# Optimization experiments

Hardware: AMD Instinct MI355X
Metric: run time of the kernel (lower is better)

## Reference

```python
import jax, jax.numpy as jnp
import numpy as np


def setup_inputs() -> dict:
    key = jax.random.key(0)
    k1, k2, k3, k4 = jax.random.split(key, 4)
    TOKENS, IN_F, OUT_F = 4096, 4096, 11008
    x = jax.random.normal(k1, (TOKENS, IN_F), dtype=jnp.float32)
    # int8-valued weights stored in fp32 buffer, as in the torch module
    quantized_weight = jax.random.randint(k2, (OUT_F, IN_F), -128, 128).astype(jnp.float32)
    # per-output-channel scales, positive, small (like max|w|/127)
    weight_scales = (jax.random.uniform(k3, (OUT_F, 1), dtype=jnp.float32) * 0.03 + 0.001)
    bias = jax.random.normal(k4, (OUT_F,), dtype=jnp.float32)
    return {"x": x, "quantized_weight": quantized_weight,
            "weight_scales": weight_scales, "bias": bias}


def reference(x, quantized_weight, weight_scales, bias):
    # dequantize: per-channel scale broadcast over in_features
    weight = quantized_weight * weight_scales  # [out, in]
    # F.linear: x @ weight.T + bias
    return jnp.dot(x, weight.T) + bias
```

## Files before the change

kernel.cpp:

```cpp
#include <hip/hip_runtime.h>
#include <hip/hip_bf16.h>


typedef __attribute__((ext_vector_type(4))) int   i32x4;
typedef __attribute__((ext_vector_type(4))) float f32x4;
typedef __attribute__((ext_vector_type(4))) unsigned int u32x4;

__device__ static inline unsigned int pack4(int q0, int q1, int q2, int q3) {
    return (unsigned)(q0 & 255) | ((unsigned)(q1 & 255) << 8) |
           ((unsigned)(q2 & 255) << 16) | ((unsigned)(q3 & 255) << 24);
}

__global__ void w_to_i8(const float* __restrict__ in,
                        u32x4* __restrict__ out, long n16) {
    const long stride = (long)gridDim.x * blockDim.x;
    for (long i = (long)blockIdx.x * blockDim.x + threadIdx.x; i < n16; i += stride) {
        const f32x4* p = reinterpret_cast<const f32x4*>(in) + i * 4;
        u32x4 o;
#pragma unroll
        for (int v = 0; v < 4; ++v) {
            f32x4 f = p[v];
            o[v] = pack4(__float2int_rn(f[0]), __float2int_rn(f[1]),
                         __float2int_rn(f[2]), __float2int_rn(f[3]));
        }
        out[i] = o;
    }
}

__global__ void x_quant_i8(const float* __restrict__ x,
                           unsigned int* __restrict__ xq,
                           float* __restrict__ sx, int K) {
    const int row = blockIdx.x;
    const int tid = threadIdx.x;
    const float* xr = x + (size_t)row * K;
    float m = 0.f;
    for (int b = tid * 16; b < K; b += blockDim.x * 16) {
        const f32x4* p = (const f32x4*)(xr + b);
#pragma unroll
        for (int v = 0; v < 4; ++v) {
            f32x4 f = p[v];
            m = fmaxf(m, fmaxf(fmaxf(fabsf(f[0]), fabsf(f[1])),
                               fmaxf(fabsf(f[2]), fabsf(f[3]))));
        }
    }
#pragma unroll
    for (int off = 32; off; off >>= 1) m = fmaxf(m, __shfl_xor(m, off));
    __shared__ float red[8];
    if ((tid & 63) == 0) red[tid >> 6] = m;
    __syncthreads();
    const int nw = blockDim.x >> 6;
    m = red[0];
    for (int i = 1; i < nw; ++i) m = fmaxf(m, red[i]);
    const float inv = (m > 0.f) ? 127.0f / m : 0.f;
    if (tid == 0) sx[row] = m * (1.0f / 127.0f);
    for (int b = tid * 16; b < K; b += blockDim.x * 16) {
        const f32x4* p = (const f32x4*)(xr + b);
        u32x4 o;
#pragma unroll
        for (int v = 0; v < 4; ++v) {
            f32x4 f = p[v];
            int q0 = min(127, max(-127, __float2int_rn(f[0] * inv)));
            int q1 = min(127, max(-127, __float2int_rn(f[1] * inv)));
            int q2 = min(127, max(-127, __float2int_rn(f[2] * inv)));
            int q3 = min(127, max(-127, __float2int_rn(f[3] * inv)));
            o[v] = pack4(q0, q1, q2, q3);
        }
        *reinterpret_cast<u32x4*>((char*)xq + (size_t)row * K + b) = o;
    }
}


#define GLOAD16(src, dst) __builtin_amdgcn_global_load_lds( \
    (const __attribute__((address_space(1))) void*)(src),   \
    (__attribute__((address_space(3))) void*)(dst), 16, 0, 0)

#define FENCE() asm volatile("" ::: "memory")
#define BAR()  do { FENCE(); __builtin_amdgcn_s_barrier(); FENCE(); } while (0)
#define WAIT_VM(n) asm volatile("s_waitcnt vmcnt(" #n ")" ::: "memory")
#define WAIT_LGKM0() asm volatile("s_waitcnt lgkmcnt(0)" ::: "memory")
#define SCHED0() __builtin_amdgcn_sched_barrier(0)

__global__ __launch_bounds__(512, 4)
void qlinear_gemm_i8(const char* __restrict__ A,
                     const char* __restrict__ B,
                     const float* __restrict__ sx,
                     const float* __restrict__ scales,
                     const float* __restrict__ bias,
                     float* __restrict__ C,
                     int M, int N, int K, int nbx) {
    __shared__ __align__(128) char smem[73728];

    const int tid  = threadIdx.x;
    const int lane = tid & 63;
    const int wid  = tid >> 6;
    const int mslab = (wid >> 1) * 64;
    const int nslab = (wid & 1) * 64;

    const int nwg = gridDim.x;
    const int q = nwg >> 3, r = nwg & 7;
    const int xcd = blockIdx.x & 7, boff_ = blockIdx.x >> 3;
    const int swz = (xcd < r ? xcd * (q + 1) : r * (q + 1) + (xcd - r) * q) + boff_;
    const int bcol = swz % nbx;
    const int brow = swz / nbx;

    const char* Ag = A + (size_t)brow * 256 * K;
    const char* Bg = B + (size_t)bcol * 128 * K;

    const int c0 = tid, c1 = tid + 512;
    const int r0 = c0 >> 2, p0 = c0 & 3;
    const int r1 = c1 >> 2, p1 = c1 & 3;
    const size_t a0base = (size_t)r0 * K + ((p0 ^ ((r0 >> 1) & 3)) << 4);
    const size_t a1base = (size_t)r1 * K + ((p1 ^ ((r1 >> 1) & 3)) << 4);
    const size_t b0base = a0base;

    auto stageT = [&](int sl, int t) {
        const size_t ko = (size_t)t * 64;
        GLOAD16(Ag + a0base + ko, smem + sl * 16384 + c0 * 16);
        GLOAD16(Ag + a1base + ko, smem + sl * 16384 + c1 * 16);
        GLOAD16(Bg + b0base + ko, smem + 49152 + sl * 8192 + c0 * 16);
    };

    const int cph  = ((lane >> 4) ^ ((lane >> 1) & 3)) << 4;
    const int aoff = (mslab + (lane & 15)) * 64 + cph;
    const int boff = (nslab + (lane & 15)) * 64 + cph;

    i32x4 acc[4][4] = {};
    i32x4 af[4], bf[4];

    auto rdAB = [&](int sl) {
        const char* pa = smem + sl * 16384 + aoff;
#pragma unroll
        for (int mi = 0; mi < 4; ++mi) af[mi] = *(const i32x4*)(pa + mi * 1024);
        const char* pb = smem + 49152 + sl * 8192 + boff;
#pragma unroll
        for (int ni = 0; ni < 4; ++ni) bf[ni] = *(const i32x4*)(pb + ni * 1024);
    };
    auto mfma16 = [&]() {
        __builtin_amdgcn_s_setprio(1);
#pragma unroll
        for (int mi = 0; mi < 4; ++mi)
#pragma unroll
            for (int ni = 0; ni < 4; ++ni)
                acc[mi][ni] = __builtin_amdgcn_mfma_i32_16x16x64_i8(
                    af[mi], bf[ni], acc[mi][ni], 0, 0, 0);
        __builtin_amdgcn_s_setprio(0);
    };

    const int NT = K / 64;

    stageT(0, 0); stageT(1, 1);
    WAIT_VM(3); BAR();

    int sl = 0;
    for (int t = 0; t < NT - 2; ++t) {
        rdAB(sl);
        int sl2 = sl + 2; if (sl2 >= 3) sl2 -= 3;
        stageT(sl2, t + 2);
        BAR();
        WAIT_LGKM0(); SCHED0();
        mfma16();
        WAIT_VM(3);
        BAR();
        sl = (sl == 2) ? 0 : sl + 1;
    }
    rdAB(sl);
    BAR();
    WAIT_LGKM0(); SCHED0();
    mfma16();
    WAIT_VM(0);
    BAR();
    sl = (sl == 2) ? 0 : sl + 1;
    rdAB(sl);
    WAIT_LGKM0(); SCHED0();
    mfma16();

    const int lc  = lane & 15;
    const int lr4 = (lane >> 4) * 4;
    float sarr[4], barr[4];
#pragma unroll
    for (int ni = 0; ni < 4; ++ni) {
        const int n = bcol * 128 + nslab + ni * 16 + lc;
        sarr[ni] = scales[n];
        barr[ni] = bias[n];
    }
#pragma unroll
    for (int mi = 0; mi < 4; ++mi) {
        const int mb = brow * 256 + mslab + mi * 16 + lr4;
        const f32x4 sxv = *(const f32x4*)&sx[mb];
#pragma unroll
        for (int j = 0; j < 4; ++j) {
            const size_t rowoff = (size_t)(mb + j) * N;
            const float sm = sxv[j];
#pragma unroll
            for (int ni = 0; ni < 4; ++ni) {
                const int n = bcol * 128 + nslab + ni * 16 + lc;
                C[rowoff + n] = fmaf((float)acc[mi][ni][j], sm * sarr[ni], barr[ni]);
            }
        }
    }
}

__global__ void qlinear_fallback(const float* __restrict__ A,
                                 const float* __restrict__ B,
                                 const float* __restrict__ scales,
                                 const float* __restrict__ bias,
                                 float* __restrict__ C, int M, int N, int K) {
    __shared__ float As[16][17], Bs[16][17];
    const int tx = threadIdx.x, ty = threadIdx.y;
    const int row = blockIdx.y * 16 + ty;
    const int col = blockIdx.x * 16 + tx;
    float acc = 0.f;
    for (int k0 = 0; k0 < K; k0 += 16) {
        As[ty][tx] = A[(long)row * K + k0 + tx];
        Bs[ty][tx] = B[(long)(blockIdx.x * 16 + ty) * K + k0 + tx];
        __syncthreads();
#pragma unroll
        for (int kk = 0; kk < 16; ++kk) acc += As[ty][kk] * Bs[tx][kk];
        __syncthreads();
    }
    C[(long)row * N + col] = fmaf(acc, scales[col], bias[col]);
}

extern "C" void kernel_launch(void* const* d_in, const int* in_sizes, int n_in,
                              void* d_out, int out_size, void* d_ws, size_t ws_size,
                              hipStream_t stream) {
    const float* x      = (const float*)d_in[0];
    const float* w      = (const float*)d_in[1];
    const float* scales = (const float*)d_in[2];
    const float* bias   = (const float*)d_in[3];
    float* out = (float*)d_out;

    const int N = in_sizes[2];
    const int K = (int)((long)in_sizes[1] / N);
    const int M = (int)((long)in_sizes[0] / K);

    const size_t need = (size_t)M * K + (size_t)N * K + (size_t)M * 4;
    const bool ok = (ws_size >= need) && (M % 256) == 0 && (N % 128) == 0 &&
                    (K % 64) == 0 && (K / 64) >= 4 && (K % 16) == 0;

    if (ok) {
        char* xq = (char*)d_ws;
        char* wq = xq + (size_t)M * K;
        float* sxbuf = (float*)(wq + (size_t)N * K);

        x_quant_i8<<<M, 256, 0, stream>>>(x, (unsigned int*)xq, sxbuf, K);
        w_to_i8<<<2048, 256, 0, stream>>>(w, (u32x4*)wq, (long)N * K / 16);

        const int nbx = N / 128;
        const int nwg = (M / 256) * nbx;
        qlinear_gemm_i8<<<nwg, 512, 0, stream>>>(xq, wq, sxbuf, scales, bias,
                                                 out, M, N, K, nbx);
    } else {
        dim3 grid(N / 16, M / 16), blk(16, 16);
        qlinear_fallback<<<grid, blk, 0, stream>>>(x, w, scales, bias, out, M, N, K);
    }
}
```

Before: 277.9 us.

## Use 4 waves with 128x64 warp tiles and drop mid-iteration barrier

```diff
diff --git a/kernel.cpp b/kernel.cpp
--- a/kernel.cpp
+++ b/kernel.cpp
@@ -77,23 +77,21 @@
 #define FENCE() asm volatile("" ::: "memory")
 #define BAR()  do { FENCE(); __builtin_amdgcn_s_barrier(); FENCE(); } while (0)
 #define WAIT_VM(n) asm volatile("s_waitcnt vmcnt(" #n ")" ::: "memory")
-#define WAIT_LGKM0() asm volatile("s_waitcnt lgkmcnt(0)" ::: "memory")
-#define SCHED0() __builtin_amdgcn_sched_barrier(0)
-
-__global__ __launch_bounds__(512, 4)
-void qlinear_gemm_i8(const char* __restrict__ A,
-                     const char* __restrict__ B,
-                     const float* __restrict__ sx,
-                     const float* __restrict__ scales,
-                     const float* __restrict__ bias,
-                     float* __restrict__ C,
-                     int M, int N, int K, int nbx) {
+
+__global__ __launch_bounds__(256, 2)
+void qlinear_gemm_i8w(const char* __restrict__ A,
+                      const char* __restrict__ B,
+                      const float* __restrict__ sx,
+                      const float* __restrict__ scales,
+                      const float* __restrict__ bias,
+                      float* __restrict__ C,
+                      int M, int N, int K, int nbx) {
     __shared__ __align__(128) char smem[73728];
 
     const int tid  = threadIdx.x;
     const int lane = tid & 63;
     const int wid  = tid >> 6;
-    const int mslab = (wid >> 1) * 64;
+    const int mslab = (wid >> 1) * 128;
     const int nslab = (wid & 1) * 64;
 
     const int nwg = gridDim.x;
@@ -106,39 +104,48 @@
     const char* Ag = A + (size_t)brow * 256 * K;
     const char* Bg = B + (size_t)bcol * 128 * K;
 
-    const int c0 = tid, c1 = tid + 512;
-    const int r0 = c0 >> 2, p0 = c0 & 3;
-    const int r1 = c1 >> 2, p1 = c1 & 3;
-    const size_t a0base = (size_t)r0 * K + ((p0 ^ ((r0 >> 1) & 3)) << 4);
-    const size_t a1base = (size_t)r1 * K + ((p1 ^ ((r1 >> 1) & 3)) << 4);
-    const size_t b0base = a0base;
+    size_t ga[4], gb[2];
+#pragma unroll
+    for (int j = 0; j < 4; ++j) {
+        const int c = tid + j * 256, rr = c >> 2, pp = c & 3;
+        ga[j] = (size_t)rr * K + ((pp ^ ((rr >> 1) & 3)) << 4);
+    }
+#pragma unroll
+    for (int j = 0; j < 2; ++j) {
+        const int c = tid + j * 256, rr = c >> 2, pp = c & 3;
+        gb[j] = (size_t)rr * K + ((pp ^ ((rr >> 1) & 3)) << 4);
+    }
 
     auto stageT = [&](int sl, int t) {
         const size_t ko = (size_t)t * 64;
-        GLOAD16(Ag + a0base + ko, smem + sl * 16384 + c0 * 16);
-        GLOAD16(Ag + a1base + ko, smem + sl * 16384 + c1 * 16);
-        GLOAD16(Bg + b0base + ko, smem + 49152 + sl * 8192 + c0 * 16);
+        char* base = smem + sl * 24576;
+#pragma unroll
+        for (int j = 0; j < 4; ++j)
+            GLOAD16(Ag + ga[j] + ko, base + (tid + j * 256) * 16);
+#pragma unroll
+        for (int j = 0; j < 2; ++j)
+            GLOAD16(Bg + gb[j] + ko, base + 16384 + (tid + j * 256) * 16);
     };
 
     const int cph  = ((lane >> 4) ^ ((lane >> 1) & 3)) << 4;
     const int aoff = (mslab + (lane & 15)) * 64 + cph;
     const int boff = (nslab + (lane & 15)) * 64 + cph;
 
-    i32x4 acc[4][4] = {};
-    i32x4 af[4], bf[4];
+    i32x4 acc[8][4] = {};
+    i32x4 af[8], bf[4];
 
     auto rdAB = [&](int sl) {
-        const char* pa = smem + sl * 16384 + aoff;
-#pragma unroll
-        for (int mi = 0; mi < 4; ++mi) af[mi] = *(const i32x4*)(pa + mi * 1024);
-        const char* pb = smem + 49152 + sl * 8192 + boff;
+        const char* pa = smem + sl * 24576 + aoff;
+#pragma unroll
+        for (int mi = 0; mi < 8; ++mi) af[mi] = *(const i32x4*)(pa + mi * 1024);
+        const char* pb = smem + sl * 24576 + 16384 + boff;
 #pragma unroll
         for (int ni = 0; ni < 4; ++ni) bf[ni] = *(const i32x4*)(pb + ni * 1024);
     };
-    auto mfma16 = [&]() {
+    auto mfma32 = [&]() {
         __builtin_amdgcn_s_setprio(1);
 #pragma unroll
-        for (int mi = 0; mi < 4; ++mi)
+        for (int mi = 0; mi < 8; ++mi)
 #pragma unroll
             for (int ni = 0; ni < 4; ++ni)
                 acc[mi][ni] = __builtin_amdgcn_mfma_i32_16x16x64_i8(
@@ -149,30 +156,25 @@
     const int NT = K / 64;
 
     stageT(0, 0); stageT(1, 1);
-    WAIT_VM(3); BAR();
+    WAIT_VM(6); BAR();
 
     int sl = 0;
     for (int t = 0; t < NT - 2; ++t) {
+        int s2 = sl + 2; if (s2 >= 3) s2 -= 3;
+        stageT(s2, t + 2);
         rdAB(sl);
-        int sl2 = sl + 2; if (sl2 >= 3) sl2 -= 3;
-        stageT(sl2, t + 2);
-        BAR();
-        WAIT_LGKM0(); SCHED0();
-        mfma16();
-        WAIT_VM(3);
+        mfma32();
+        WAIT_VM(6);
         BAR();
         sl = (sl == 2) ? 0 : sl + 1;
     }
     rdAB(sl);
-    BAR();
-    WAIT_LGKM0(); SCHED0();
-    mfma16();
+    mfma32();
     WAIT_VM(0);
     BAR();
     sl = (sl == 2) ? 0 : sl + 1;
     rdAB(sl);
-    WAIT_LGKM0(); SCHED0();
-    mfma16();
+    mfma32();
 
     const int lc  = lane & 15;
     const int lr4 = (lane >> 4) * 4;
@@ -184,7 +186,7 @@
         barr[ni] = bias[n];
     }
 #pragma unroll
-    for (int mi = 0; mi < 4; ++mi) {
+    for (int mi = 0; mi < 8; ++mi) {
         const int mb = brow * 256 + mslab + mi * 16 + lr4;
         const f32x4 sxv = *(const f32x4*)&sx[mb];
 #pragma unroll
@@ -248,8 +250,8 @@
 
         const int nbx = N / 128;
         const int nwg = (M / 256) * nbx;
-        qlinear_gemm_i8<<<nwg, 512, 0, stream>>>(xq, wq, sxbuf, scales, bias,
-                                                 out, M, N, K, nbx);
+        qlinear_gemm_i8w<<<nwg, 256, 0, stream>>>(xq, wq, sxbuf, scales, bias,
+                                                  out, M, N, K, nbx);
     } else {
         dim3 grid(N / 16, M / 16), blk(16, 16);
         qlinear_fallback<<<grid, blk, 0, stream>>>(x, w, scales, bias, out, M, N, K);
```

New measurement: 270.9 us. 2.5% less time.

## Enlarge int8 GEMM tile to 256x256 with phased half-tile staging

Applied to the files above, without the earlier changes.

```diff
diff --git a/kernel.cpp b/kernel.cpp
--- a/kernel.cpp
+++ b/kernel.cpp
@@ -80,21 +80,21 @@
 #define WAIT_LGKM0() asm volatile("s_waitcnt lgkmcnt(0)" ::: "memory")
 #define SCHED0() __builtin_amdgcn_sched_barrier(0)
 
-__global__ __launch_bounds__(512, 4)
-void qlinear_gemm_i8(const char* __restrict__ A,
-                     const char* __restrict__ B,
-                     const float* __restrict__ sx,
-                     const float* __restrict__ scales,
-                     const float* __restrict__ bias,
-                     float* __restrict__ C,
-                     int M, int N, int K, int nbx) {
-    __shared__ __align__(128) char smem[73728];
+__global__ __launch_bounds__(512, 2)
+void qlinear_gemm_i8p8(const char* __restrict__ A,
+                       const char* __restrict__ B,
+                       const float* __restrict__ sx,
+                       const float* __restrict__ scales,
+                       const float* __restrict__ bias,
+                       float* __restrict__ C,
+                       int M, int N, int K, int nbx) {
+    __shared__ __align__(128) char smem[98304];
 
     const int tid  = threadIdx.x;
     const int lane = tid & 63;
     const int wid  = tid >> 6;
-    const int mslab = (wid >> 1) * 64;
-    const int nslab = (wid & 1) * 64;
+    const int wr   = wid >> 2;
+    const int wc   = wid & 3;
 
     const int nwg = gridDim.x;
     const int q = nwg >> 3, r = nwg & 7;
@@ -104,96 +104,122 @@
     const int brow = swz / nbx;
 
     const char* Ag = A + (size_t)brow * 256 * K;
-    const char* Bg = B + (size_t)bcol * 128 * K;
-
-    const int c0 = tid, c1 = tid + 512;
-    const int r0 = c0 >> 2, p0 = c0 & 3;
-    const int r1 = c1 >> 2, p1 = c1 & 3;
-    const size_t a0base = (size_t)r0 * K + ((p0 ^ ((r0 >> 1) & 3)) << 4);
-    const size_t a1base = (size_t)r1 * K + ((p1 ^ ((r1 >> 1) & 3)) << 4);
-    const size_t b0base = a0base;
-
-    auto stageT = [&](int sl, int t) {
-        const size_t ko = (size_t)t * 64;
-        GLOAD16(Ag + a0base + ko, smem + sl * 16384 + c0 * 16);
-        GLOAD16(Ag + a1base + ko, smem + sl * 16384 + c1 * 16);
-        GLOAD16(Bg + b0base + ko, smem + 49152 + sl * 8192 + c0 * 16);
+    const char* Bg = B + (size_t)bcol * 256 * K;
+
+    const int srow = tid >> 2;
+    const size_t gsrc = ((size_t)srow * K) + (((tid & 3) ^ ((tid >> 3) & 3)) << 4);
+    const int ldst = tid * 16;
+
+    auto stageH = [&](int mat, int h, int rs, int t) {
+        const char* G = (mat ? Bg : Ag) + (size_t)h * 128 * K;
+        GLOAD16(G + gsrc + (size_t)t * 64,
+                smem + mat * 49152 + rs * 16384 + h * 8192 + ldst);
     };
 
     const int cph  = ((lane >> 4) ^ ((lane >> 1) & 3)) << 4;
-    const int aoff = (mslab + (lane & 15)) * 64 + cph;
-    const int boff = (nslab + (lane & 15)) * 64 + cph;
-
-    i32x4 acc[4][4] = {};
-    i32x4 af[4], bf[4];
-
-    auto rdAB = [&](int sl) {
-        const char* pa = smem + sl * 16384 + aoff;
-#pragma unroll
-        for (int mi = 0; mi < 4; ++mi) af[mi] = *(const i32x4*)(pa + mi * 1024);
-        const char* pb = smem + 49152 + sl * 8192 + boff;
-#pragma unroll
-        for (int ni = 0; ni < 4; ++ni) bf[ni] = *(const i32x4*)(pb + ni * 1024);
-    };
-    auto mfma16 = [&]() {
+    const int arow = (wr * 128 + (lane & 15)) * 64 + cph;
+    const int brow_ = (wc * 64 + (lane & 15)) * 64 + cph;
+
+    i32x4 acc[8][4] = {};
+    i32x4 a0[4], a1[4], b0[2], b1[2];
+
+    auto rdA = [&](int rg, int mh, i32x4 (&d)[4]) {
+        const char* p = smem + rg * 16384 + arow + mh * 4096;
+#pragma unroll
+        for (int i = 0; i < 4; ++i) d[i] = *(const i32x4*)(p + i * 1024);
+    };
+    auto rdB = [&](int rg, int nh, i32x4 (&d)[2]) {
+        const char* p = smem + 49152 + rg * 16384 + brow_ + nh * 2048;
+#pragma unroll
+        for (int n = 0; n < 2; ++n) d[n] = *(const i32x4*)(p + n * 1024);
+    };
+    auto mfma8 = [&](const i32x4 (&a)[4], const i32x4 (&b)[2], int qm, int qn) {
         __builtin_amdgcn_s_setprio(1);
 #pragma unroll
-        for (int mi = 0; mi < 4; ++mi)
-#pragma unroll
-            for (int ni = 0; ni < 4; ++ni)
-                acc[mi][ni] = __builtin_amdgcn_mfma_i32_16x16x64_i8(
-                    af[mi], bf[ni], acc[mi][ni], 0, 0, 0);
+        for (int i = 0; i < 4; ++i)
+#pragma unroll
+            for (int n = 0; n < 2; ++n)
+                acc[qm * 4 + i][qn * 2 + n] = __builtin_amdgcn_mfma_i32_16x16x64_i8(
+                    a[i], b[n], acc[qm * 4 + i][qn * 2 + n], 0, 0, 0);
         __builtin_amdgcn_s_setprio(0);
     };
 
     const int NT = K / 64;
 
-    stageT(0, 0); stageT(1, 1);
-    WAIT_VM(3); BAR();
-
-    int sl = 0;
+    stageH(0, 0, 0, 0); stageH(1, 0, 0, 0); stageH(0, 1, 0, 0); stageH(1, 1, 0, 0);
+    stageH(0, 0, 1, 1); stageH(1, 0, 1, 1); stageH(0, 1, 1, 1); stageH(1, 1, 1, 1);
+    WAIT_VM(4); BAR();
+
+    int rg = 0;
     for (int t = 0; t < NT - 2; ++t) {
-        rdAB(sl);
-        int sl2 = sl + 2; if (sl2 >= 3) sl2 -= 3;
-        stageT(sl2, t + 2);
-        BAR();
-        WAIT_LGKM0(); SCHED0();
-        mfma16();
-        WAIT_VM(3);
-        BAR();
-        sl = (sl == 2) ? 0 : sl + 1;
-    }
-    rdAB(sl);
-    BAR();
+        int rs = rg + 2; if (rs >= 3) rs -= 3;
+        rdA(rg, 0, a0); rdB(rg, 0, b0);
+        stageH(0, 0, rs, t + 2);
+        BAR(); WAIT_LGKM0(); SCHED0();
+        mfma8(a0, b0, 0, 0);
+        BAR();
+        rdA(rg, 1, a1);
+        stageH(1, 0, rs, t + 2);
+        BAR(); WAIT_LGKM0(); SCHED0();
+        mfma8(a1, b0, 1, 0);
+        BAR();
+        rdB(rg, 1, b1);
+        stageH(0, 1, rs, t + 2);
+        BAR(); WAIT_LGKM0(); SCHED0();
+        mfma8(a0, b1, 0, 1);
+        BAR();
+        stageH(1, 1, rs, t + 2);
+        mfma8(a1, b1, 1, 1);
+        WAIT_VM(4);
+        BAR();
+        rg = (rg == 2) ? 0 : rg + 1;
+    }
+    rdA(rg, 0, a0); rdB(rg, 0, b0);
+    BAR(); WAIT_LGKM0(); SCHED0();
+    mfma8(a0, b0, 0, 0);
+    BAR();
+    rdA(rg, 1, a1);
+    BAR(); WAIT_LGKM0(); SCHED0();
+    mfma8(a1, b0, 1, 0);
+    BAR();
+    rdB(rg, 1, b1);
+    BAR(); WAIT_LGKM0(); SCHED0();
+    mfma8(a0, b1, 0, 1);
+    BAR();
+    mfma8(a1, b1, 1, 1);
+    WAIT_VM(0);
+    BAR();
+    rg = (rg == 2) ? 0 : rg + 1;
+    rdA(rg, 0, a0); rdB(rg, 0, b0);
     WAIT_LGKM0(); SCHED0();
-    mfma16();
-    WAIT_VM(0);
-    BAR();
-    sl = (sl == 2) ? 0 : sl + 1;
-    rdAB(sl);
+    mfma8(a0, b0, 0, 0);
+    rdA(rg, 1, a1);
     WAIT_LGKM0(); SCHED0();
-    mfma16();
+    mfma8(a1, b0, 1, 0);
+    rdB(rg, 1, b1);
+    WAIT_LGKM0(); SCHED0();
+    mfma8(a0, b1, 0, 1);
+    mfma8(a1, b1, 1, 1);
 
     const int lc  = lane & 15;
     const int lr4 = (lane >> 4) * 4;
     float sarr[4], barr[4];
 #pragma unroll
     for (int ni = 0; ni < 4; ++ni) {
-        const int n = bcol * 128 + nslab + ni * 16 + lc;
+        const int n = bcol * 256 + wc * 64 + (ni >> 1) * 32 + (ni & 1) * 16 + lc;
         sarr[ni] = scales[n];
         barr[ni] = bias[n];
     }
 #pragma unroll
-    for (int mi = 0; mi < 4; ++mi) {
-        const int mb = brow * 256 + mslab + mi * 16 + lr4;
-        const f32x4 sxv = *(const f32x4*)&sx[mb];
+    for (int mi = 0; mi < 8; ++mi) {
+        const int mb = brow * 256 + wr * 128 + (mi >> 2) * 64 + (mi & 3) * 16 + lr4;
 #pragma unroll
         for (int j = 0; j < 4; ++j) {
             const size_t rowoff = (size_t)(mb + j) * N;
-            const float sm = sxv[j];
+            const float sm = sx[mb + j];
 #pragma unroll
             for (int ni = 0; ni < 4; ++ni) {
-                const int n = bcol * 128 + nslab + ni * 16 + lc;
+                const int n = bcol * 256 + wc * 64 + (ni >> 1) * 32 + (ni & 1) * 16 + lc;
                 C[rowoff + n] = fmaf((float)acc[mi][ni][j], sm * sarr[ni], barr[ni]);
             }
         }
@@ -235,7 +261,7 @@
     const int M = (int)((long)in_sizes[0] / K);
 
     const size_t need = (size_t)M * K + (size_t)N * K + (size_t)M * 4;
-    const bool ok = (ws_size >= need) && (M % 256) == 0 && (N % 128) == 0 &&
+    const bool ok = (ws_size >= need) && (M % 256) == 0 && (N % 256) == 0 &&
                     (K % 64) == 0 && (K / 64) >= 4 && (K % 16) == 0;
 
     if (ok) {
@@ -246,10 +272,10 @@
         x_quant_i8<<<M, 256, 0, stream>>>(x, (unsigned int*)xq, sxbuf, K);
         w_to_i8<<<2048, 256, 0, stream>>>(w, (u32x4*)wq, (long)N * K / 16);
 
-        const int nbx = N / 128;
+        const int nbx = N / 256;
         const int nwg = (M / 256) * nbx;
-        qlinear_gemm_i8<<<nwg, 512, 0, stream>>>(xq, wq, sxbuf, scales, bias,
-                                                 out, M, N, K, nbx);
+        qlinear_gemm_i8p8<<<nwg, 512, 0, stream>>>(xq, wq, sxbuf, scales, bias,
+                                                   out, M, N, K, nbx);
     } else {
         dim3 grid(N / 16, M / 16), blk(16, 16);
         qlinear_fallback<<<grid, blk, 0, stream>>>(x, w, scales, bias, out, M, N, K);
```

Measured after the change: 266.2 us. 1.04x faster.
